# Kernel tuning notes

Hardware: AMD Instinct MI355X
Metric: run time of the kernel (lower is better)

Reference implementation:

```python
import jax, jax.numpy as jnp
import numpy as np

GAMMA = 20.0
GAMMA2 = 10.0
KATZ_FACTOR = 0.5
EPS = 1e-8


def setup_inputs() -> dict:
    key = jax.random.key(0)
    k1, k2, k3, k4 = jax.random.split(key, 4)
    b, n_way, k_shot, q, c, h, w = 16, 5, 5, 75, 640, 5, 5
    return {
        "support_xf": jax.random.normal(k1, (b, n_way * k_shot, c, h, w), jnp.float32),
        "support_y": jax.random.randint(k2, (b, n_way * k_shot), 0, n_way),
        "query_xf": jax.random.normal(k3, (b, q, c, h, w), jnp.float32),
        "query_y": jax.random.randint(k4, (b, q), 0, n_way),
        "n_way": n_way,
        "k_shot": k_shot,
    }


def _mel_loss(support_xf, query_xf, query_y, n_way, k_shot):
    b, s, c, h, w = support_xf.shape
    q = query_xf.shape[1]
    hw = h * w
    # averaging-based similarities: mean over shots, cosine over channel dim
    sup = support_xf.reshape(b, n_way, k_shot, c, hw).mean(2)          # (b, n_way, c, hw)
    sup = sup / (jnp.linalg.norm(sup, axis=2, keepdims=True) + EPS)
    qry = query_xf.reshape(b, q, c, hw)                                 # (b, q, c, hw)
    qry = qry / (jnp.linalg.norm(qry, axis=2, keepdims=True) + EPS)
    # S[b,q,way,i,j] = cos(query pixel i, support pixel j)
    S = jnp.einsum('bqci,bwcj->bqwij', qry, sup)                        # (b, q, n_way, hw, hw)
    M_q = hw
    M_s = n_way * hw
    S = S.transpose(0, 1, 3, 2, 4).reshape(b * q, M_q, M_s)             # (N, M_q, M_s)
    N = b * q

    # gamma-scaled softmax transition matrices
    T_sq = jax.nn.softmax(GAMMA * S, axis=-1)                           # (N, M_q, M_s)
    T_qs = jax.nn.softmax(GAMMA2 * jnp.swapaxes(S, -1, -2), axis=-1)    # (N, M_s, M_q)

    # bipartite block transition matrix T (N, M_s+M_q, M_s+M_q)
    top = jnp.concatenate([jnp.zeros((N, M_s, M_s), S.dtype),
                           jnp.swapaxes(T_sq, -1, -2)], axis=-1)
    bot = jnp.concatenate([jnp.swapaxes(T_qs, -1, -2),
                           jnp.zeros((N, M_q, M_q), S.dtype)], axis=-1)
    T = jnp.concatenate([top, bot], axis=-2)

    # katz = (inv(I - a*T) - I) @ 1  ==  solve(I - a*T, 1) - 1
    A = jnp.eye(M_s + M_q, dtype=S.dtype) - KATZ_FACTOR * T
    ones = jnp.ones((N, M_s + M_q, 1), S.dtype)
    katz = jnp.linalg.solve(A, ones)[..., 0] - 1.0                      # (N, M_s+M_q)

    pk = katz[:, :M_s]
    pk = pk / pk.sum(-1, keepdims=True)
    predicts = pk.reshape(N, n_way, -1).sum(-1)                         # (N, n_way)

    yv = query_y.reshape(N)
    logp = jnp.log(predicts)
    loss = -jnp.mean(logp[jnp.arange(N), yv])                           # NLLLoss
    return loss


def reference(support_xf, support_y, query_xf, query_y, n_way, k_shot):
    return _mel_loss(support_xf, query_xf, query_y, n_way, k_shot)
```

## Files before the change

kernel.cpp:

```cpp
#include <hip/hip_runtime.h>
#include <hip/hip_bf16.h>
#include <math.h>

#define NN   1200
#define EPSF 1e-8f

typedef __attribute__((ext_vector_type(8)))  short bf8v;
typedef __attribute__((ext_vector_type(16))) float f16v;

static __device__ inline ushort f2bf(float v) {
  __hip_bfloat16 b = __float2bfloat16(v);
  return *reinterpret_cast<ushort*>(&b);
}
static __device__ inline float bf2f(ushort u) {
  union { unsigned x; float f; } c; c.x = ((unsigned)u) << 16; return c.f;
}

__global__ __launch_bounds__(256) void kA(const float* __restrict__ sxf,
                                          ushort* __restrict__ sup) {
  const int blk = blockIdx.x;
  const int b = blk / 5, w = blk % 5;
  const int tid = threadIdx.x;
  __shared__ __align__(16) float slab[25 * 641];
  __shared__ float rinv[25];
  const float* base = sxf + (size_t)blk * 5 * 16000;

  for (int f0 = tid * 4; f0 < 16000; f0 += 1024) {
    float4 a  = *(const float4*)(base + f0);
    float4 b1 = *(const float4*)(base + 16000 + f0);
    float4 c1 = *(const float4*)(base + 32000 + f0);
    float4 d1 = *(const float4*)(base + 48000 + f0);
    float4 e1 = *(const float4*)(base + 64000 + f0);
    float v[4];
    v[0] = (a.x + b1.x + c1.x + d1.x + e1.x) * 0.2f;
    v[1] = (a.y + b1.y + c1.y + d1.y + e1.y) * 0.2f;
    v[2] = (a.z + b1.z + c1.z + d1.z + e1.z) * 0.2f;
    v[3] = (a.w + b1.w + c1.w + d1.w + e1.w) * 0.2f;
#pragma unroll
    for (int u = 0; u < 4; ++u) {
      int f = f0 + u, j = f % 25, c = f / 25;
      slab[j * 641 + c] = v[u];
    }
  }
  __syncthreads();
  if (tid < 200) {
    int i = tid >> 3, l = tid & 7;
    float ssq = 0.f;
    for (int c = l; c < 640; c += 8) { float v = slab[i * 641 + c]; ssq = fmaf(v, v, ssq); }
    ssq += __shfl_xor(ssq, 1, 8);
    ssq += __shfl_xor(ssq, 2, 8);
    ssq += __shfl_xor(ssq, 4, 8);
    if (l == 0) rinv[i] = 1.f / (sqrtf(ssq) + EPSF);
  }
  __syncthreads();
  for (int g0 = tid * 4; g0 < 16000; g0 += 1024) {
    int j = g0 / 640, c = g0 % 640;
    float r = rinv[j];
    ushort h[4], lo[4];
#pragma unroll
    for (int u = 0; u < 4; ++u) {
      float v = slab[j * 641 + c + u] * r;
      h[u] = f2bf(v);
      lo[u] = f2bf(v - bf2f(h[u]));
    }
    size_t o = (size_t)b * 160000 + (size_t)(w * 25 + j) * 640 + c;
    uint2 ph = { (unsigned)h[0] | ((unsigned)h[1] << 16), (unsigned)h[2] | ((unsigned)h[3] << 16) };
    uint2 pl = { (unsigned)lo[0] | ((unsigned)lo[1] << 16), (unsigned)lo[2] | ((unsigned)lo[3] << 16) };
    *(uint2*)(sup + o) = ph;
    *(uint2*)(sup + o + 80000) = pl;
  }
}

__global__ __launch_bounds__(256, 3) void kC(const float* __restrict__ qxf,
                                             const int* __restrict__ qy,
                                             const ushort* __restrict__ sup,
                                             float* __restrict__ out) {
  const int n = blockIdx.x;
  const int b = n / 75;
  const int tid = threadIdx.x;
  const int lane = tid & 63;
  const int hi32 = lane >> 5;
  const int wv = tid >> 6;
  __shared__ __align__(16) char stage[46080];
  __shared__ float nsq[25], rinv[25], rhs[25], xv[25], Pk[5];

  const float* qb = qxf + (size_t)n * 16000;
  const ushort* supb = sup + (size_t)b * 160000;

  { unsigned* sd = (unsigned*)stage;
    for (int i = tid; i < 11520; i += 256) sd[i] = 0u; }
  if (tid < 25) nsq[tid] = 0.f;
  if (tid < 5)  Pk[tid] = 0.f;
  __syncthreads();

  f16v acc;
#pragma unroll
  for (int r = 0; r < 16; ++r) acc[r] = 0.f;
  const int arow = lane & 31;
  const int brow = wv * 32 + (lane & 31);

  for (int ch = 0; ch < 10; ++ch) {
    const int k0 = ch * 64;
    for (int idx = tid; idx < 400; idx += 256) {
      int row = idx >> 4, c4 = idx & 15;
      float4 qv = *(const float4*)(qb + row * 640 + k0 + c4 * 4);
      atomicAdd(&nsq[row], qv.x*qv.x + qv.y*qv.y + qv.z*qv.z + qv.w*qv.w);
      ushort h[4], lo[4];
      float vv[4] = { qv.x, qv.y, qv.z, qv.w };
#pragma unroll
      for (int u = 0; u < 4; ++u) { h[u] = f2bf(vv[u]); lo[u] = f2bf(vv[u] - bf2f(h[u])); }
      uint2 ph = { (unsigned)h[0] | ((unsigned)h[1] << 16), (unsigned)h[2] | ((unsigned)h[3] << 16) };
      uint2 pl = { (unsigned)lo[0] | ((unsigned)lo[1] << 16), (unsigned)lo[2] | ((unsigned)lo[3] << 16) };
      *(uint2*)(stage + row * 144 + c4 * 8) = ph;
      *(uint2*)(stage + 4608 + row * 144 + c4 * 8) = pl;
    }
    for (int idx = tid; idx < 2000; idx += 256) {
      int hl = (idx >= 1000) ? 1 : 0;
      int r2 = idx - hl * 1000;
      int row = r2 >> 3, seg = r2 & 7;
      uint4 v = *(const uint4*)(supb + hl * 80000 + row * 640 + k0 + seg * 8);
      *(uint4*)(stage + 9216 + hl * 18432 + row * 144 + seg * 16) = v;
    }
    __syncthreads();
#pragma unroll
    for (int ks = 0; ks < 4; ++ks) {
      const int kb2 = ks * 32 + hi32 * 16;
      bf8v ah = *(const bf8v*)(stage + arow * 144 + kb2);
      bf8v al = *(const bf8v*)(stage + 4608 + arow * 144 + kb2);
      bf8v bh = *(const bf8v*)(stage + 9216 + brow * 144 + kb2);
      bf8v bl = *(const bf8v*)(stage + 27648 + brow * 144 + kb2);
      acc = __builtin_amdgcn_mfma_f32_32x32x16_bf16(ah, bh, acc, 0, 0, 0);
      acc = __builtin_amdgcn_mfma_f32_32x32x16_bf16(al, bh, acc, 0, 0, 0);
      acc = __builtin_amdgcn_mfma_f32_32x32x16_bf16(ah, bl, acc, 0, 0, 0);
    }
    __syncthreads();
  }

  if (tid < 25) rinv[tid] = 1.f / (sqrtf(nsq[tid]) + EPSF);
  __syncthreads();

  float* Sm = (float*)(stage + 30720);
  { const int col = wv * 32 + (lane & 31);
#pragma unroll
    for (int r = 0; r < 16; ++r) {
      int row = (r & 3) + 8 * (r >> 2) + 4 * hi32;
      if (row < 25 && col < 125) Sm[row * 125 + col] = acc[r] * rinv[row];
    }
  }
  __syncthreads();

  float* Tsq  = (float*)stage;
  float* TqsT = (float*)(stage + 12800);
  float* Bm   = (float*)(stage + 25600);

  if (tid < 200) {
    int i = tid >> 3, l = tid & 7;
    const float* Srow = Sm + i * 125;
    float mx = -1e30f;
    for (int ss = l; ss < 125; ss += 8) mx = fmaxf(mx, Srow[ss]);
    mx = fmaxf(mx, __shfl_xor(mx, 1, 8));
    mx = fmaxf(mx, __shfl_xor(mx, 2, 8));
    mx = fmaxf(mx, __shfl_xor(mx, 4, 8));
    float sm = 0.f;
    for (int ss = l; ss < 128; ss += 8) {
      float e = 0.f;
      if (ss < 125) { e = __expf(20.f * (Srow[ss] - mx)); sm += e; }
      Tsq[i * 128 + ss] = e;
    }
    sm += __shfl_xor(sm, 1, 8);
    sm += __shfl_xor(sm, 2, 8);
    sm += __shfl_xor(sm, 4, 8);
    float rs = 1.f / sm;
    for (int ss = l; ss < 125; ss += 8) Tsq[i * 128 + ss] *= rs;
  }
  if (tid < 125) {
    int ss = tid;
    float mx = -1e30f;
#pragma unroll
    for (int i = 0; i < 25; ++i) mx = fmaxf(mx, Sm[i * 125 + ss]);
    float sm = 0.f;
    float ev[25];
#pragma unroll
    for (int i = 0; i < 25; ++i) { ev[i] = __expf(10.f * (Sm[i * 125 + ss] - mx)); sm += ev[i]; }
    float rs = 1.f / sm;
#pragma unroll
    for (int i = 0; i < 25; ++i) TqsT[i * 128 + ss] = ev[i] * rs;
  }
  if (tid < 25) { TqsT[tid * 128 + 125] = 0.f; TqsT[tid * 128 + 126] = 0.f; TqsT[tid * 128 + 127] = 0.f; }
  __syncthreads();

  for (int ii = tid; ii < 625; ii += 256) {
    int i = ii / 25, ip = ii % 25;
    const float* ta = TqsT + i * 128;
    const float* tb = Tsq + ip * 128;
    float4 s4 = { 0.f, 0.f, 0.f, 0.f };
#pragma unroll
    for (int q4 = 0; q4 < 32; ++q4) {
      float4 a4 = *(const float4*)(ta + q4 * 4);
      float4 b4 = *(const float4*)(tb + q4 * 4);
      s4.x = fmaf(a4.x, b4.x, s4.x); s4.y = fmaf(a4.y, b4.y, s4.y);
      s4.z = fmaf(a4.z, b4.z, s4.z); s4.w = fmaf(a4.w, b4.w, s4.w);
    }
    Bm[i * 25 + ip] = (s4.x + s4.y) + (s4.z + s4.w);
  }
  if (tid < 25) {
    const float* ta = TqsT + tid * 128;
    float4 s4 = { 0.f, 0.f, 0.f, 0.f };
#pragma unroll
    for (int q4 = 0; q4 < 32; ++q4) {
      float4 a4 = *(const float4*)(ta + q4 * 4);
      s4.x += a4.x; s4.y += a4.y; s4.z += a4.z; s4.w += a4.w;
    }
    rhs[tid] = 1.f + 0.5f * ((s4.x + s4.y) + (s4.z + s4.w));
  }
  __syncthreads();

  if (tid < 64) {
    float Brow[25], x, rh;
    if (tid < 25) {
      rh = rhs[tid]; x = rh;
#pragma unroll
      for (int ip = 0; ip < 25; ++ip) Brow[ip] = Bm[tid * 25 + ip];
    } else {
      rh = 0.f; x = 0.f;
#pragma unroll
      for (int ip = 0; ip < 25; ++ip) Brow[ip] = 0.f;
    }
#pragma unroll
    for (int it = 0; it < 16; ++it) {
      float sum = 0.f;
#pragma unroll
      for (int ip = 0; ip < 25; ++ip) sum = fmaf(Brow[ip], __shfl(x, ip), sum);
      x = rh + 0.25f * sum;
    }
    if (tid < 25) xv[tid] = x;
  }
  __syncthreads();

  if (tid < 125) {
    float kz = 0.f;
#pragma unroll
    for (int i = 0; i < 25; ++i) kz = fmaf(Tsq[i * 128 + tid], xv[i], kz);
    atomicAdd(&Pk[tid / 25], kz);
  }
  __syncthreads();
  if (tid == 0) {
    float den = Pk[0] + Pk[1] + Pk[2] + Pk[3] + Pk[4];
    int y = qy[n];
    float v = -(logf(Pk[y]) - logf(den)) * (1.0f / (float)NN);
    atomicAdd(out, v);
  }
}

extern "C" void kernel_launch(void* const* d_in, const int* in_sizes, int n_in,
                              void* d_out, int out_size, void* d_ws, size_t ws_size,
                              hipStream_t stream) {
  const float* sxf = (const float*)d_in[0];
  const float* qxf = (const float*)d_in[2];
  const int*   qy  = (const int*)d_in[3];
  float* out = (float*)d_out;
  ushort* sup = (ushort*)d_ws;

  hipMemsetAsync(out, 0, sizeof(float), stream);
  kA<<<80, 256, 0, stream>>>(sxf, sup);
  kC<<<NN, 256, 0, stream>>>(qxf, qy, sup, out);
}
```

Measured before the change: 297.6 us.

## Split pipeline into four kernels, share support tiles across two queries

New measurement: 251.5 us. 1.18x faster.

```diff
diff --git a/kernel.cpp b/kernel.cpp
--- a/kernel.cpp
+++ b/kernel.cpp
@@ -16,146 +16,209 @@
   union { unsigned x; float f; } c; c.x = ((unsigned)u) << 16; return c.f;
 }
 
-__global__ __launch_bounds__(256) void kA(const float* __restrict__ sxf,
-                                          ushort* __restrict__ sup) {
+__global__ __launch_bounds__(256) void kA1(const float* __restrict__ sxf,
+                                           float* __restrict__ supmean) {
   const int blk = blockIdx.x;
-  const int b = blk / 5, w = blk % 5;
+  const int b = blk / 25, rem = blk % 25, w = rem / 5, ck = rem % 5;
+  const int c0 = ck * 128;
   const int tid = threadIdx.x;
-  __shared__ __align__(16) float slab[25 * 641];
-  __shared__ float rinv[25];
-  const float* base = sxf + (size_t)blk * 5 * 16000;
-
-  for (int f0 = tid * 4; f0 < 16000; f0 += 1024) {
+  __shared__ float lds[3200];
+  const float* base = sxf + (size_t)(b * 25 + w * 5) * 16000 + (size_t)c0 * 25;
+
+  for (int f0 = tid * 4; f0 < 3200; f0 += 1024) {
     float4 a  = *(const float4*)(base + f0);
     float4 b1 = *(const float4*)(base + 16000 + f0);
     float4 c1 = *(const float4*)(base + 32000 + f0);
     float4 d1 = *(const float4*)(base + 48000 + f0);
     float4 e1 = *(const float4*)(base + 64000 + f0);
-    float v[4];
-    v[0] = (a.x + b1.x + c1.x + d1.x + e1.x) * 0.2f;
-    v[1] = (a.y + b1.y + c1.y + d1.y + e1.y) * 0.2f;
-    v[2] = (a.z + b1.z + c1.z + d1.z + e1.z) * 0.2f;
-    v[3] = (a.w + b1.w + c1.w + d1.w + e1.w) * 0.2f;
-#pragma unroll
-    for (int u = 0; u < 4; ++u) {
-      int f = f0 + u, j = f % 25, c = f / 25;
-      slab[j * 641 + c] = v[u];
-    }
-  }
-  __syncthreads();
-  if (tid < 200) {
-    int i = tid >> 3, l = tid & 7;
-    float ssq = 0.f;
-    for (int c = l; c < 640; c += 8) { float v = slab[i * 641 + c]; ssq = fmaf(v, v, ssq); }
-    ssq += __shfl_xor(ssq, 1, 8);
-    ssq += __shfl_xor(ssq, 2, 8);
-    ssq += __shfl_xor(ssq, 4, 8);
-    if (l == 0) rinv[i] = 1.f / (sqrtf(ssq) + EPSF);
-  }
-  __syncthreads();
-  for (int g0 = tid * 4; g0 < 16000; g0 += 1024) {
-    int j = g0 / 640, c = g0 % 640;
-    float r = rinv[j];
+    lds[f0 + 0] = (a.x + b1.x + c1.x + d1.x + e1.x) * 0.2f;
+    lds[f0 + 1] = (a.y + b1.y + c1.y + d1.y + e1.y) * 0.2f;
+    lds[f0 + 2] = (a.z + b1.z + c1.z + d1.z + e1.z) * 0.2f;
+    lds[f0 + 3] = (a.w + b1.w + c1.w + d1.w + e1.w) * 0.2f;
+  }
+  __syncthreads();
+  for (int g = tid; g < 3200; g += 256) {
+    int j = g >> 7, cc = g & 127;
+    supmean[(size_t)(b * 125 + w * 25 + j) * 640 + c0 + cc] = lds[cc * 25 + j];
+  }
+}
+
+__global__ __launch_bounds__(256) void kA2(const float* __restrict__ supmean,
+                                           ushort* __restrict__ sup) {
+  const int r = blockIdx.x * 4 + (threadIdx.x >> 6);
+  const int lane = threadIdx.x & 63;
+  const int b = r / 125, s = r % 125;
+  const float* row = supmean + (size_t)r * 640;
+  float4 v0 = *(const float4*)(row + lane * 4);
+  float4 v1 = *(const float4*)(row + 256 + lane * 4);
+  float4 v2 = {0.f, 0.f, 0.f, 0.f};
+  if (lane < 32) v2 = *(const float4*)(row + 512 + lane * 4);
+  float ssq = v0.x*v0.x + v0.y*v0.y + v0.z*v0.z + v0.w*v0.w
+            + v1.x*v1.x + v1.y*v1.y + v1.z*v1.z + v1.w*v1.w
+            + v2.x*v2.x + v2.y*v2.y + v2.z*v2.z + v2.w*v2.w;
+#pragma unroll
+  for (int d = 32; d; d >>= 1) ssq += __shfl_xor(ssq, d);
+  const float rinv = 1.f / (sqrtf(ssq) + EPSF);
+  ushort* dst = sup + (size_t)b * 160000 + (size_t)s * 640;
+#pragma unroll
+  for (int seg = 0; seg < 3; ++seg) {
+    if (seg == 2 && lane >= 32) break;
+    float4 v = (seg == 0) ? v0 : ((seg == 1) ? v1 : v2);
+    int c = seg * 256 + lane * 4;
+    float vv[4] = { v.x * rinv, v.y * rinv, v.z * rinv, v.w * rinv };
     ushort h[4], lo[4];
 #pragma unroll
-    for (int u = 0; u < 4; ++u) {
-      float v = slab[j * 641 + c + u] * r;
-      h[u] = f2bf(v);
-      lo[u] = f2bf(v - bf2f(h[u]));
-    }
-    size_t o = (size_t)b * 160000 + (size_t)(w * 25 + j) * 640 + c;
+    for (int u = 0; u < 4; ++u) { h[u] = f2bf(vv[u]); lo[u] = f2bf(vv[u] - bf2f(h[u])); }
     uint2 ph = { (unsigned)h[0] | ((unsigned)h[1] << 16), (unsigned)h[2] | ((unsigned)h[3] << 16) };
     uint2 pl = { (unsigned)lo[0] | ((unsigned)lo[1] << 16), (unsigned)lo[2] | ((unsigned)lo[3] << 16) };
-    *(uint2*)(sup + o) = ph;
-    *(uint2*)(sup + o + 80000) = pl;
-  }
-}
-
-__global__ __launch_bounds__(256, 3) void kC(const float* __restrict__ qxf,
-                                             const int* __restrict__ qy,
+    *(uint2*)(dst + c) = ph;
+    *(uint2*)(dst + 80000 + c) = pl;
+  }
+}
+
+__global__ __launch_bounds__(256, 3) void kG(const float* __restrict__ qxf,
                                              const ushort* __restrict__ sup,
-                                             float* __restrict__ out) {
-  const int n = blockIdx.x;
-  const int b = n / 75;
+                                             float* __restrict__ Sg) {
+  const int blk = blockIdx.x;
+  const int b = blk / 38, qq = blk - b * 38;
+  const int q0 = 2 * qq;
+  const int n0 = b * 75 + q0;
+  const bool has1 = (q0 + 1) < 75;
   const int tid = threadIdx.x;
-  const int lane = tid & 63;
-  const int hi32 = lane >> 5;
-  const int wv = tid >> 6;
-  __shared__ __align__(16) char stage[46080];
-  __shared__ float nsq[25], rinv[25], rhs[25], xv[25], Pk[5];
-
-  const float* qb = qxf + (size_t)n * 16000;
+  const int lane = tid & 63, hi32 = lane >> 5, wv = tid >> 6;
+  __shared__ __align__(16) char st[49152];
+  __shared__ float nsq[64], rinvs[64];
+
+  const float* qb0 = qxf + (size_t)n0 * 16000;
+  const float* qb1 = qxf + (size_t)(n0 + (has1 ? 1 : 0)) * 16000;
   const ushort* supb = sup + (size_t)b * 160000;
 
-  { unsigned* sd = (unsigned*)stage;
-    for (int i = tid; i < 11520; i += 256) sd[i] = 0u; }
-  if (tid < 25) nsq[tid] = 0.f;
-  if (tid < 5)  Pk[tid] = 0.f;
-  __syncthreads();
-
-  f16v acc;
-#pragma unroll
-  for (int r = 0; r < 16; ++r) acc[r] = 0.f;
+  if (tid < 64) nsq[tid] = 0.f;
+  __syncthreads();
+
+  f16v acc0, acc1;
+#pragma unroll
+  for (int r = 0; r < 16; ++r) { acc0[r] = 0.f; acc1[r] = 0.f; }
   const int arow = lane & 31;
   const int brow = wv * 32 + (lane & 31);
+  const int aoffs[4] = {
+    (arow * 128 + 0 * 32 + hi32 * 16) ^ ((arow & 7) << 4),
+    (arow * 128 + 1 * 32 + hi32 * 16) ^ ((arow & 7) << 4),
+    (arow * 128 + 2 * 32 + hi32 * 16) ^ ((arow & 7) << 4),
+    (arow * 128 + 3 * 32 + hi32 * 16) ^ ((arow & 7) << 4) };
+  const int boffs[4] = {
+    (brow * 128 + 0 * 32 + hi32 * 16) ^ ((brow & 7) << 4),
+    (brow * 128 + 1 * 32 + hi32 * 16) ^ ((brow & 7) << 4),
+    (brow * 128 + 2 * 32 + hi32 * 16) ^ ((brow & 7) << 4),
+    (brow * 128 + 3 * 32 + hi32 * 16) ^ ((brow & 7) << 4) };
 
   for (int ch = 0; ch < 10; ++ch) {
     const int k0 = ch * 64;
-    for (int idx = tid; idx < 400; idx += 256) {
-      int row = idx >> 4, c4 = idx & 15;
+    for (int idx = tid; idx < 800; idx += 256) {
+      int qs = (idx >= 400) ? 1 : 0;
+      int r2 = idx - qs * 400;
+      int row = r2 >> 4, c4 = r2 & 15;
+      const float* qb = qs ? qb1 : qb0;
       float4 qv = *(const float4*)(qb + row * 640 + k0 + c4 * 4);
-      atomicAdd(&nsq[row], qv.x*qv.x + qv.y*qv.y + qv.z*qv.z + qv.w*qv.w);
+      float ssq = qv.x*qv.x + qv.y*qv.y + qv.z*qv.z + qv.w*qv.w;
+      ssq += __shfl_xor(ssq, 1, 16);
+      ssq += __shfl_xor(ssq, 2, 16);
+      ssq += __shfl_xor(ssq, 4, 16);
+      ssq += __shfl_xor(ssq, 8, 16);
       ushort h[4], lo[4];
       float vv[4] = { qv.x, qv.y, qv.z, qv.w };
 #pragma unroll
       for (int u = 0; u < 4; ++u) { h[u] = f2bf(vv[u]); lo[u] = f2bf(vv[u] - bf2f(h[u])); }
       uint2 ph = { (unsigned)h[0] | ((unsigned)h[1] << 16), (unsigned)h[2] | ((unsigned)h[3] << 16) };
       uint2 pl = { (unsigned)lo[0] | ((unsigned)lo[1] << 16), (unsigned)lo[2] | ((unsigned)lo[3] << 16) };
-      *(uint2*)(stage + row * 144 + c4 * 8) = ph;
-      *(uint2*)(stage + 4608 + row * 144 + c4 * 8) = pl;
+      int off = (row * 128 + c4 * 8) ^ ((row & 7) << 4);
+      *(uint2*)(st + qs * 8192 + off) = ph;
+      *(uint2*)(st + qs * 8192 + 4096 + off) = pl;
+      if ((r2 & 15) == 0) nsq[qs * 32 + row] += ssq;
     }
     for (int idx = tid; idx < 2000; idx += 256) {
       int hl = (idx >= 1000) ? 1 : 0;
       int r2 = idx - hl * 1000;
       int row = r2 >> 3, seg = r2 & 7;
       uint4 v = *(const uint4*)(supb + hl * 80000 + row * 640 + k0 + seg * 8);
-      *(uint4*)(stage + 9216 + hl * 18432 + row * 144 + seg * 16) = v;
+      int off = (row * 128 + seg * 16) ^ ((row & 7) << 4);
+      *(uint4*)(st + 16384 + hl * 16384 + off) = v;
     }
     __syncthreads();
 #pragma unroll
     for (int ks = 0; ks < 4; ++ks) {
-      const int kb2 = ks * 32 + hi32 * 16;
-      bf8v ah = *(const bf8v*)(stage + arow * 144 + kb2);
-      bf8v al = *(const bf8v*)(stage + 4608 + arow * 144 + kb2);
-      bf8v bh = *(const bf8v*)(stage + 9216 + brow * 144 + kb2);
-      bf8v bl = *(const bf8v*)(stage + 27648 + brow * 144 + kb2);
-      acc = __builtin_amdgcn_mfma_f32_32x32x16_bf16(ah, bh, acc, 0, 0, 0);
-      acc = __builtin_amdgcn_mfma_f32_32x32x16_bf16(al, bh, acc, 0, 0, 0);
-      acc = __builtin_amdgcn_mfma_f32_32x32x16_bf16(ah, bl, acc, 0, 0, 0);
+      bf8v bh  = *(const bf8v*)(st + 16384 + boffs[ks]);
+      bf8v bl  = *(const bf8v*)(st + 32768 + boffs[ks]);
+      bf8v ah0 = *(const bf8v*)(st + aoffs[ks]);
+      bf8v al0 = *(const bf8v*)(st + 4096 + aoffs[ks]);
+      bf8v ah1 = *(const bf8v*)(st + 8192 + aoffs[ks]);
+      bf8v al1 = *(const bf8v*)(st + 12288 + aoffs[ks]);
+      acc0 = __builtin_amdgcn_mfma_f32_32x32x16_bf16(ah0, bh, acc0, 0, 0, 0);
+      acc0 = __builtin_amdgcn_mfma_f32_32x32x16_bf16(al0, bh, acc0, 0, 0, 0);
+      acc0 = __builtin_amdgcn_mfma_f32_32x32x16_bf16(ah0, bl, acc0, 0, 0, 0);
+      acc1 = __builtin_amdgcn_mfma_f32_32x32x16_bf16(ah1, bh, acc1, 0, 0, 0);
+      acc1 = __builtin_amdgcn_mfma_f32_32x32x16_bf16(al1, bh, acc1, 0, 0, 0);
+      acc1 = __builtin_amdgcn_mfma_f32_32x32x16_bf16(ah1, bl, acc1, 0, 0, 0);
     }
     __syncthreads();
   }
 
-  if (tid < 25) rinv[tid] = 1.f / (sqrtf(nsq[tid]) + EPSF);
-  __syncthreads();
-
-  float* Sm = (float*)(stage + 30720);
-  { const int col = wv * 32 + (lane & 31);
-#pragma unroll
-    for (int r = 0; r < 16; ++r) {
-      int row = (r & 3) + 8 * (r >> 2) + 4 * hi32;
-      if (row < 25 && col < 125) Sm[row * 125 + col] = acc[r] * rinv[row];
-    }
-  }
-  __syncthreads();
-
-  float* Tsq  = (float*)stage;
-  float* TqsT = (float*)(stage + 12800);
-  float* Bm   = (float*)(stage + 25600);
-
+  if (tid < 64) rinvs[tid] = 1.f / (sqrtf(nsq[tid]) + EPSF);
+  __syncthreads();
+
+  const int col = wv * 32 + (lane & 31);
+  float* So0 = Sg + (size_t)n0 * 3200;
+  float* So1 = So0 + 3200;
+#pragma unroll
+  for (int r = 0; r < 16; ++r) {
+    int row = (r & 3) + 8 * (r >> 2) + 4 * hi32;
+    if (row < 25) {
+      So0[row * 128 + col] = acc0[r] * rinvs[row];
+      if (has1) So1[row * 128 + col] = acc1[r] * rinvs[32 + row];
+    }
+  }
+}
+
+#define LD 132
+__global__ __launch_bounds__(256, 4) void kT(const float* __restrict__ Sg,
+                                             const int* __restrict__ qy,
+                                             float* __restrict__ out) {
+  const int n = blockIdx.x;
+  const int tid = threadIdx.x;
+  __shared__ __align__(16) float S[25 * LD];
+  __shared__ __align__(16) float TqsT[25 * LD];
+  __shared__ float Bm[625], rhs[25], xv[25], Pk[5];
+
+  const float* sgn = Sg + (size_t)n * 3200;
+  for (int idx = tid; idx < 800; idx += 256) {
+    int row = idx >> 5, q4 = idx & 31;
+    *(float4*)(S + row * LD + q4 * 4) = *(const float4*)(sgn + row * 128 + q4 * 4);
+  }
+  if (tid < 5) Pk[tid] = 0.f;
+  if (tid >= 32 && tid < 57) {
+    int i = tid - 32;
+    TqsT[i * LD + 125] = 0.f; TqsT[i * LD + 126] = 0.f; TqsT[i * LD + 127] = 0.f;
+  }
+  __syncthreads();
+
+  if (tid < 125) {
+    float mx = -1e30f;
+#pragma unroll
+    for (int i = 0; i < 25; ++i) mx = fmaxf(mx, S[i * LD + tid]);
+    float sm = 0.f;
+#pragma unroll
+    for (int i = 0; i < 25; ++i) {
+      float e = __expf(10.f * (S[i * LD + tid] - mx));
+      TqsT[i * LD + tid] = e; sm += e;
+    }
+    float rs = 1.f / sm;
+#pragma unroll
+    for (int i = 0; i < 25; ++i) TqsT[i * LD + tid] *= rs;
+  }
+  __syncthreads();
   if (tid < 200) {
     int i = tid >> 3, l = tid & 7;
-    const float* Srow = Sm + i * 125;
+    float* Srow = S + i * LD;
     float mx = -1e30f;
     for (int ss = l; ss < 125; ss += 8) mx = fmaxf(mx, Srow[ss]);
     mx = fmaxf(mx, __shfl_xor(mx, 1, 8));
@@ -165,34 +228,20 @@
     for (int ss = l; ss < 128; ss += 8) {
       float e = 0.f;
       if (ss < 125) { e = __expf(20.f * (Srow[ss] - mx)); sm += e; }
-      Tsq[i * 128 + ss] = e;
+      Srow[ss] = e;
     }
     sm += __shfl_xor(sm, 1, 8);
     sm += __shfl_xor(sm, 2, 8);
     sm += __shfl_xor(sm, 4, 8);
     float rs = 1.f / sm;
-    for (int ss = l; ss < 125; ss += 8) Tsq[i * 128 + ss] *= rs;
-  }
-  if (tid < 125) {
-    int ss = tid;
-    float mx = -1e30f;
-#pragma unroll
-    for (int i = 0; i < 25; ++i) mx = fmaxf(mx, Sm[i * 125 + ss]);
-    float sm = 0.f;
-    float ev[25];
-#pragma unroll
-    for (int i = 0; i < 25; ++i) { ev[i] = __expf(10.f * (Sm[i * 125 + ss] - mx)); sm += ev[i]; }
-    float rs = 1.f / sm;
-#pragma unroll
-    for (int i = 0; i < 25; ++i) TqsT[i * 128 + ss] = ev[i] * rs;
-  }
-  if (tid < 25) { TqsT[tid * 128 + 125] = 0.f; TqsT[tid * 128 + 126] = 0.f; TqsT[tid * 128 + 127] = 0.f; }
+    for (int ss = l; ss < 125; ss += 8) Srow[ss] *= rs;
+  }
   __syncthreads();
 
   for (int ii = tid; ii < 625; ii += 256) {
     int i = ii / 25, ip = ii % 25;
-    const float* ta = TqsT + i * 128;
-    const float* tb = Tsq + ip * 128;
+    const float* ta = TqsT + i * LD;
+    const float* tb = S + ip * LD;
     float4 s4 = { 0.f, 0.f, 0.f, 0.f };
 #pragma unroll
     for (int q4 = 0; q4 < 32; ++q4) {
@@ -201,10 +250,10 @@
       s4.x = fmaf(a4.x, b4.x, s4.x); s4.y = fmaf(a4.y, b4.y, s4.y);
       s4.z = fmaf(a4.z, b4.z, s4.z); s4.w = fmaf(a4.w, b4.w, s4.w);
     }
-    Bm[i * 25 + ip] = (s4.x + s4.y) + (s4.z + s4.w);
+    Bm[ii] = (s4.x + s4.y) + (s4.z + s4.w);
   }
   if (tid < 25) {
-    const float* ta = TqsT + tid * 128;
+    const float* ta = TqsT + tid * LD;
     float4 s4 = { 0.f, 0.f, 0.f, 0.f };
 #pragma unroll
     for (int q4 = 0; q4 < 32; ++q4) {
@@ -240,7 +289,7 @@
   if (tid < 125) {
     float kz = 0.f;
 #pragma unroll
-    for (int i = 0; i < 25; ++i) kz = fmaf(Tsq[i * 128 + tid], xv[i], kz);
+    for (int i = 0; i < 25; ++i) kz = fmaf(S[i * LD + tid], xv[i], kz);
     atomicAdd(&Pk[tid / 25], kz);
   }
   __syncthreads();
@@ -259,9 +308,13 @@
   const float* qxf = (const float*)d_in[2];
   const int*   qy  = (const int*)d_in[3];
   float* out = (float*)d_out;
-  ushort* sup = (ushort*)d_ws;
+  float*  supmean = (float*)d_ws;
+  ushort* sup     = (ushort*)((char*)d_ws + 5120000);
+  float*  Sgw     = (float*)((char*)d_ws + 10240000);
 
   hipMemsetAsync(out, 0, sizeof(float), stream);
-  kA<<<80, 256, 0, stream>>>(sxf, sup);
-  kC<<<NN, 256, 0, stream>>>(qxf, qy, sup, out);
-}
+  kA1<<<400, 256, 0, stream>>>(sxf, supmean);
+  kA2<<<500, 256, 0, stream>>>(supmean, sup);
+  kG<<<608, 256, 0, stream>>>(qxf, sup, Sgw);
+  kT<<<NN, 256, 0, stream>>>(Sgw, qy, out);
+}
```
